# Optimization experiments

Hardware: AMD Instinct MI355X
Metric: run time of the kernel (lower is better)

Reference implementation:

```python
import jax, jax.numpy as jnp
import numpy as np

N = 50000   # nodes
E = 800000  # edges (avg degree 16)
D = 128     # dim (in == out per layer)
R = 8       # num_relations
B = 4       # num_bases
L = 2       # conv_layer_num
EPS = 1e-5      # LayerNorm eps
SLOPE = 0.2     # leaky_relu negative slope


def setup_inputs() -> dict:
    key = jax.random.key(0)
    ks = jax.random.split(key, 10)
    s = 0.05
    x = jax.random.normal(ks[0], (N, D), dtype=jnp.float32)
    edge_index = jax.random.randint(ks[1], (2, E), 0, N)
    edge_type = jax.random.randint(ks[2], (E,), 0, R)
    basis = jax.random.normal(ks[3], (L, B, D, D), dtype=jnp.float32) * s
    att_r = jax.random.normal(ks[4], (L, R, B), dtype=jnp.float32) * s
    att = jax.random.normal(ks[5], (L, 2 * D), dtype=jnp.float32) * s
    root = jax.random.normal(ks[6], (L, D, D), dtype=jnp.float32) * s
    bias = jax.random.normal(ks[7], (L, D), dtype=jnp.float32) * s
    ln_w = jnp.ones((L, D), dtype=jnp.float32)
    ln_b = jnp.zeros((L, D), dtype=jnp.float32)
    return {"x": x, "edge_index": edge_index, "edge_type": edge_type,
            "basis": basis, "att_r": att_r, "att": att, "root": root,
            "bias": bias, "ln_w": ln_w, "ln_b": ln_b}


def _gnn_layer(x, src, dst, et, basis, att_r, att, root, bias, ln_w, ln_b):
    # relation weights from bases: [R, D, D]
    w = jnp.einsum('rb,bio->rio', att_r, basis)
    # transform all nodes under all relations once, then gather per edge
    xw = jnp.einsum('ni,rio->rno', x, w)          # [R, N, D]
    x_j = xw[et, src]                              # [E, D] relation-specific src msg
    xr = x @ root                                  # [N, D] root transform
    x_i = xr[dst]                                  # [E, D]
    # attention: (cat[x_i, x_j] * att).sum(-1), leaky_relu, segment softmax by dst
    alpha = x_i @ att[:D] + x_j @ att[D:]          # [E]
    alpha = jnp.where(alpha > 0, alpha, SLOPE * alpha)
    amax = jax.ops.segment_max(alpha, dst, num_segments=N)
    amax = jnp.where(jnp.isfinite(amax), amax, 0.0)
    ex = jnp.exp(alpha - amax[dst])
    denom = jax.ops.segment_sum(ex, dst, num_segments=N)
    alpha = ex / (denom[dst] + 1e-16)
    # weighted scatter-add aggregation (dropout rate = 0 -> identity)
    aggr = jax.ops.segment_sum(x_j * alpha[:, None], dst, num_segments=N)  # [N, D]
    out = aggr + xr + bias
    # LayerNorm
    mu = out.mean(-1, keepdims=True)
    var = out.var(-1, keepdims=True)
    out = (out - mu) / jnp.sqrt(var + EPS) * ln_w + ln_b
    return jnp.tanh(out)


def reference(x, edge_index, edge_type, basis, att_r, att, root, bias, ln_w, ln_b):
    src, dst = edge_index[0], edge_index[1]
    states = []
    for l in range(L):
        x = _gnn_layer(x, src, dst, edge_type, basis[l], att_r[l], att[l],
                       root[l], bias[l], ln_w[l], ln_b[l])
        states.append(x)
    return (x, jnp.stack(states))
```

## Files before the change

kernel.cpp:

```cpp
#include <hip/hip_runtime.h>
#include <math.h>

#define D 128
#define NB 4
#define NR 8
#define NLAYER 2
#define KTOT 640
#define EPSV 1e-5f
#define SLOPE 0.2f
#define NBUK 32
#define BSHIFT 11

typedef __attribute__((ext_vector_type(8))) short short8;
typedef __attribute__((ext_vector_type(4))) float f32x4;

__device__ __forceinline__ unsigned short f2bf(float f) {
  unsigned u = __float_as_uint(f);
  u += 0x7FFF + ((u >> 16) & 1);
  return (unsigned short)(u >> 16);
}

__device__ __forceinline__ float block_sum_128(float v, volatile float* scratch) {
#pragma unroll
  for (int off = 32; off > 0; off >>= 1) v += __shfl_xor(v, off);
  __syncthreads();
  if ((threadIdx.x & 63) == 0) scratch[threadIdx.x >> 6] = v;
  __syncthreads();
  return scratch[0] + scratch[1];
}

__global__ void hist_kernel(const int* __restrict__ dst, int* __restrict__ deg, int E) {
  int e = blockIdx.x * 256 + threadIdx.x;
  if (e < E) atomicAdd(&deg[dst[e]], 1);
}

__global__ void __launch_bounds__(1024) scan_kernel(const int* __restrict__ deg,
                                                    int* __restrict__ offs,
                                                    int* __restrict__ cur,
                                                    int* __restrict__ bcur, int n) {
  __shared__ int wsums[16];
  const int tid = threadIdx.x, lane = tid & 63, wid = tid >> 6;
  int carry = 0;
  for (int base = 0; base < n; base += 4096) {
    int i0 = base + tid * 4;
    int v0 = 0, v1 = 0, v2 = 0, v3 = 0;
    if (i0 + 3 < n) {
      int4 q = *(const int4*)(deg + i0);
      v0 = q.x; v1 = q.y; v2 = q.z; v3 = q.w;
    } else if (i0 < n) {
      v0 = deg[i0];
      if (i0 + 1 < n) v1 = deg[i0 + 1];
      if (i0 + 2 < n) v2 = deg[i0 + 2];
    }
    int tsum = v0 + v1 + v2 + v3;
    int x = tsum;
#pragma unroll
    for (int off = 1; off < 64; off <<= 1) {
      int y = __shfl_up(x, off);
      if (lane >= off) x += y;
    }
    if (lane == 63) wsums[wid] = x;
    __syncthreads();
    if (wid == 0) {
      int ws = (lane < 16) ? wsums[lane] : 0;
#pragma unroll
      for (int off = 1; off < 16; off <<= 1) {
        int y = __shfl_up(ws, off);
        if (lane >= off) ws += y;
      }
      if (lane < 16) wsums[lane] = ws;
    }
    __syncthreads();
    int prefix = carry + ((wid > 0) ? wsums[wid - 1] : 0) + x - tsum;
    int e0 = prefix, e1 = e0 + v0, e2 = e1 + v1, e3 = e2 + v2;
    if (i0 < n)     { offs[i0] = e0;     cur[i0] = e0; }
    if (i0 + 1 < n) { offs[i0 + 1] = e1; cur[i0 + 1] = e1; }
    if (i0 + 2 < n) { offs[i0 + 2] = e2; cur[i0 + 2] = e2; }
    if (i0 + 3 < n) { offs[i0 + 3] = e3; cur[i0 + 3] = e3; }
    int btot = wsums[15];
    __syncthreads();
    carry += btot;
  }
  if (tid == 0) offs[n] = carry;
  __syncthreads();
  if (tid < NBUK) {
    int idx = tid << BSHIFT;
    bcur[tid * 16] = offs[idx < n ? idx : n];
  }
}

__global__ void __launch_bounds__(1024) bucket_kernel(
    const int* __restrict__ src, const int* __restrict__ dst, const int* __restrict__ et,
    int* __restrict__ bcur, unsigned long long* __restrict__ ebuf, int E) {
  __shared__ int lcnt[NBUK];
  __shared__ int lbase[NBUK];
  const int tid = threadIdx.x;
  const int e = blockIdx.x * 1024 + tid;
  if (tid < NBUK) lcnt[tid] = 0;
  __syncthreads();
  int d = 0, b = 0, rank = 0;
  unsigned pk = 0;
  bool valid = e < E;
  if (valid) {
    d = dst[e];
    pk = (unsigned)src[e] | ((unsigned)et[e] << 16);
    b = d >> BSHIFT;
    rank = atomicAdd(&lcnt[b], 1);
  }
  __syncthreads();
  if (tid < NBUK && lcnt[tid] > 0) lbase[tid] = atomicAdd(&bcur[tid * 16], lcnt[tid]);
  __syncthreads();
  if (valid) ebuf[lbase[b] + rank] = ((unsigned long long)(unsigned)d << 32) | pk;
}

__global__ void scatter2_kernel(const unsigned long long* __restrict__ ebuf,
                                int* __restrict__ cur, unsigned* __restrict__ csr, int E) {
  int e = blockIdx.x * 256 + threadIdx.x;
  if (e < E) {
    unsigned long long r = ebuf[e];
    int d = (int)(r >> 32);
    int pos = atomicAdd(&cur[d], 1);
    csr[pos] = (unsigned)r;
  }
}

__global__ void __launch_bounds__(128) prep_w(const float* __restrict__ basis,
                                              const float* __restrict__ root,
                                              const float* __restrict__ att,
                                              unsigned short* __restrict__ BT0,
                                              unsigned short* __restrict__ BT1,
                                              float* __restrict__ av0, float* __restrict__ av1) {
  __shared__ float scratch[2];
  int k = blockIdx.x, l = 0;
  if (k >= KTOT) { k -= KTOT; l = 1; }
  const float* basis_l = basis + (size_t)l * NB * D * D;
  const float* root_l  = root + (size_t)l * D * D;
  const float* att_l   = att + (size_t)l * 2 * D;
  unsigned short* BT = l ? BT1 : BT0;
  float* av = l ? av1 : av0;
  const int o = threadIdx.x;
  float v = (k < 512) ? basis_l[(size_t)(k >> 7) * (D * D) + (size_t)(k & 127) * D + o]
                      : root_l[(size_t)(k - 512) * D + o];
  BT[(size_t)o * KTOT + k] = f2bf(v);
  float w = (k < 512) ? att_l[D + o] : att_l[o];
  float s = block_sum_128(v * w, scratch);
  if (o == 0) av[k] = s;
}

__global__ void __launch_bounds__(256) prep_xa(const float* __restrict__ x0,
                                               const float* __restrict__ av,
                                               unsigned short* __restrict__ ga,
                                               float* __restrict__ ai,
                                               float* __restrict__ ajb, int N, int Npad) {
  int n = blockIdx.x * 4 + (threadIdx.x >> 6);
  int lane = threadIdx.x & 63;
  if (n >= Npad) return;
  if (n >= N) {
    *(unsigned*)(ga + (size_t)n * KTOT + 512 + 2 * lane) = 0;
    return;
  }
  float2 xv = *(const float2*)(x0 + (size_t)n * D + 2 * lane);
  unsigned packed = (unsigned)f2bf(xv.x) | ((unsigned)f2bf(xv.y) << 16);
  *(unsigned*)(ga + (size_t)n * KTOT + 512 + 2 * lane) = packed;
  float d[5];
#pragma unroll
  for (int b = 0; b < 4; ++b) {
    float2 w = *(const float2*)(av + b * D + 2 * lane);
    d[b] = xv.x * w.x + xv.y * w.y;
  }
  {
    float2 w = *(const float2*)(av + 512 + 2 * lane);
    d[4] = xv.x * w.x + xv.y * w.y;
  }
#pragma unroll
  for (int off = 1; off < 64; off <<= 1) {
#pragma unroll
    for (int i = 0; i < 5; ++i) d[i] += __shfl_xor(d[i], off);
  }
  if (lane == 0) {
    *(float4*)(ajb + (size_t)n * 4) = make_float4(d[0], d[1], d[2], d[3]);
    ai[n] = d[4];
  }
}

__global__ void __launch_bounds__(256) a2_kernel(const unsigned short* __restrict__ ga,
                                                 const float* __restrict__ av,
                                                 float* __restrict__ ai,
                                                 float* __restrict__ ajb, int N) {
  int n = blockIdx.x * 4 + (threadIdx.x >> 6);
  int lane = threadIdx.x & 63;
  if (n >= N) return;
  unsigned xv = *(const unsigned*)(ga + (size_t)n * KTOT + 512 + 2 * lane);
  float x0 = __uint_as_float(xv << 16);
  float x1 = __uint_as_float(xv & 0xFFFF0000u);
  float d[5];
#pragma unroll
  for (int b = 0; b < 4; ++b) {
    float2 w = *(const float2*)(av + b * D + 2 * lane);
    d[b] = x0 * w.x + x1 * w.y;
  }
  {
    float2 w = *(const float2*)(av + 512 + 2 * lane);
    d[4] = x0 * w.x + x1 * w.y;
  }
#pragma unroll
  for (int off = 1; off < 64; off <<= 1) {
#pragma unroll
    for (int i = 0; i < 5; ++i) d[i] += __shfl_xor(d[i], off);
  }
  if (lane == 0) {
    *(float4*)(ajb + (size_t)n * 4) = make_float4(d[0], d[1], d[2], d[3]);
    ai[n] = d[4];
  }
}

__global__ void __launch_bounds__(256) node_flash(
    unsigned short* __restrict__ ga, const float* __restrict__ ai, const float* __restrict__ ajb,
    const int* __restrict__ offs, const unsigned* __restrict__ csr,
    const float* __restrict__ attr_l, int N) {
  __shared__ float s_c[NR * NB];
  __shared__ float4 s_wc[4][64];
  __shared__ unsigned s_pk[4][64];
  const int w = threadIdx.x >> 6, lane = threadIdx.x & 63;
  const int n = blockIdx.x * 4 + w;
  if (lane < NR * NB) s_c[lane] = attr_l[lane];
  if (n >= N) return;
  const int b0 = offs[n], b1 = offs[n + 1];
  const float ain = ai[n];
  float m = -INFINITY, ssum = 0.f;
  float acc[4][2] = {};
  for (int cb = b0; cb < b1; cb += 64) {
    int cnt = min(64, b1 - cb);
    float alpha = -INFINITY;
    unsigned pk = 0;
    float4 cv = make_float4(0.f, 0.f, 0.f, 0.f);
    if (lane < cnt) {
      pk = csr[cb + lane];
      unsigned sn = pk & 0xFFFFu, rt = pk >> 16;
      float4 aj = *(const float4*)(ajb + (size_t)sn * 4);
      cv = *(const float4*)(&s_c[rt * 4]);
      float a = ain + cv.x * aj.x + cv.y * aj.y + cv.z * aj.z + cv.w * aj.w;
      alpha = a > 0.f ? a : SLOPE * a;
    }
    float cmax = alpha;
#pragma unroll
    for (int off = 32; off > 0; off >>= 1) cmax = fmaxf(cmax, __shfl_xor(cmax, off));
    float nm = fmaxf(m, cmax);
    float ex = (lane < cnt) ? __expf(alpha - nm) : 0.f;
    float csum = ex;
#pragma unroll
    for (int off = 32; off > 0; off >>= 1) csum += __shfl_xor(csum, off);
    float f = __expf(m - nm);
    ssum = ssum * f + csum;
#pragma unroll
    for (int b = 0; b < 4; ++b) { acc[b][0] *= f; acc[b][1] *= f; }
    m = nm;
    s_pk[w][lane] = pk;
    s_wc[w][lane] = make_float4(ex * cv.x, ex * cv.y, ex * cv.z, ex * cv.w);
#pragma unroll 2
    for (int j = 0; j < cnt; ++j) {
      float4 wc = s_wc[w][j];
      unsigned sn = s_pk[w][j] & 0xFFFFu;
      unsigned xv = *(const unsigned*)(ga + (size_t)sn * KTOT + 512 + 2 * lane);
      float x0 = __uint_as_float(xv << 16);
      float x1 = __uint_as_float(xv & 0xFFFF0000u);
      acc[0][0] = fmaf(wc.x, x0, acc[0][0]); acc[0][1] = fmaf(wc.x, x1, acc[0][1]);
      acc[1][0] = fmaf(wc.y, x0, acc[1][0]); acc[1][1] = fmaf(wc.y, x1, acc[1][1]);
      acc[2][0] = fmaf(wc.z, x0, acc[2][0]); acc[2][1] = fmaf(wc.z, x1, acc[2][1]);
      acc[3][0] = fmaf(wc.w, x0, acc[3][0]); acc[3][1] = fmaf(wc.w, x1, acc[3][1]);
    }
  }
  float inv = 1.f / (ssum + 1e-16f);
  unsigned short* gp = ga + (size_t)n * KTOT;
#pragma unroll
  for (int b = 0; b < 4; ++b) {
    unsigned r = (unsigned)f2bf(acc[b][0] * inv) | ((unsigned)f2bf(acc[b][1] * inv) << 16);
    *(unsigned*)(gp + b * D + 2 * lane) = r;
  }
}

__global__ void __launch_bounds__(512) gemm2_kernel(
    unsigned short* __restrict__ ga, const unsigned short* __restrict__ BT,
    const float* __restrict__ bias_l, const float* __restrict__ lnw_l,
    const float* __restrict__ lnb_l, float* __restrict__ st,
    float* __restrict__ xfinal, int n_nodes) {
  __shared__ unsigned short sB[128 * 72];
  const int tid = threadIdx.x;
  const int wv = tid >> 6, lane = tid & 63;
  const int l15 = lane & 15, quad = lane >> 4;
  const int rowb = blockIdx.x * 128 + wv * 16;
  const unsigned short* garow = ga + (size_t)(rowb + l15) * KTOT;
  f32x4 acc[8];
  const f32x4 zero = {0.f, 0.f, 0.f, 0.f};
#pragma unroll
  for (int ct = 0; ct < 8; ++ct) acc[ct] = zero;
#pragma unroll
  for (int ch = 0; ch < 10; ++ch) {
    const int k0 = ch * 64;
    short8 a[2];
#pragma unroll
    for (int kc = 0; kc < 2; ++kc)
      a[kc] = *(const short8*)(garow + k0 + kc * 32 + quad * 8);
    __syncthreads();
#pragma unroll
    for (int p = 0; p < 2; ++p) {
      int idx = p * 512 + tid;
      int col = idx >> 3, k8 = idx & 7;
      *(short8*)(sB + col * 72 + k8 * 8) =
          *(const short8*)(BT + (size_t)col * KTOT + k0 + k8 * 8);
    }
    __syncthreads();
#pragma unroll
    for (int kc = 0; kc < 2; ++kc) {
#pragma unroll
      for (int ct = 0; ct < 8; ++ct) {
        const short8* b = (const short8*)(sB + (ct * 16 + l15) * 72 + kc * 32 + quad * 8);
        acc[ct] = __builtin_amdgcn_mfma_f32_16x16x32_bf16(a[kc], *b, acc[ct], 0, 0, 0);
      }
    }
  }
  const int r0 = rowb + quad * 4;
  float bia[8], lw[8], lb[8];
#pragma unroll
  for (int ct = 0; ct < 8; ++ct) {
    int col = ct * 16 + l15;
    bia[ct] = bias_l[col]; lw[ct] = lnw_l[col]; lb[ct] = lnb_l[col];
  }
  float vsum[4] = {0.f, 0.f, 0.f, 0.f}, vsq[4] = {0.f, 0.f, 0.f, 0.f};
#pragma unroll
  for (int ct = 0; ct < 8; ++ct) {
#pragma unroll
    for (int r = 0; r < 4; ++r) {
      float v = acc[ct][r] + bia[ct];
      acc[ct][r] = v;
      vsum[r] += v; vsq[r] += v * v;
    }
  }
#pragma unroll
  for (int r = 0; r < 4; ++r) {
#pragma unroll
    for (int off = 1; off < 16; off <<= 1) {
      vsum[r] += __shfl_xor(vsum[r], off);
      vsq[r]  += __shfl_xor(vsq[r], off);
    }
  }
  float mu[4], rs[4];
#pragma unroll
  for (int r = 0; r < 4; ++r) {
    mu[r] = vsum[r] * (1.0f / D);
    float var = vsq[r] * (1.0f / D) - mu[r] * mu[r];
    rs[r] = rsqrtf(var + EPSV);
  }
#pragma unroll
  for (int ct = 0; ct < 8; ++ct) {
#pragma unroll
    for (int r = 0; r < 4; ++r) {
      int row = r0 + r;
      if (row >= n_nodes) continue;
      int col = ct * 16 + l15;
      float nv = (acc[ct][r] - mu[r]) * rs[r] * lw[ct] + lb[ct];
      float val = tanhf(nv);
      st[(size_t)row * D + col] = val;
      if (xfinal) xfinal[(size_t)row * D + col] = val;
      ga[(size_t)row * KTOT + 512 + col] = f2bf(val);
    }
  }
}

extern "C" void kernel_launch(void* const* d_in, const int* in_sizes, int n_in,
                              void* d_out, int out_size, void* d_ws, size_t ws_size,
                              hipStream_t stream) {
  const float* x0    = (const float*)d_in[0];
  const int*   ei    = (const int*)d_in[1];
  const int*   etype = (const int*)d_in[2];
  const float* basis = (const float*)d_in[3];
  const float* att_r = (const float*)d_in[4];
  const float* att   = (const float*)d_in[5];
  const float* root  = (const float*)d_in[6];
  const float* bias  = (const float*)d_in[7];
  const float* lnw   = (const float*)d_in[8];
  const float* lnb   = (const float*)d_in[9];
  float* out = (float*)d_out;
  const int N = in_sizes[0] / D;
  const int E = in_sizes[2];
  const int Npad = ((N + 127) / 128) * 128;

  char* p = (char*)d_ws;
  auto alloc = [&](size_t bytes) { void* r = (void*)p; p += (bytes + 255) & ~(size_t)255; return r; };
  unsigned short*     ga   = (unsigned short*)alloc((size_t)Npad * KTOT * 2);
  unsigned short*     BT0  = (unsigned short*)alloc((size_t)D * KTOT * 2);
  unsigned short*     BT1  = (unsigned short*)alloc((size_t)D * KTOT * 2);
  float*              av0  = (float*)alloc((size_t)KTOT * 4);
  float*              av1  = (float*)alloc((size_t)KTOT * 4);
  float*              ai   = (float*)alloc((size_t)N * 4);
  float*              ajb  = (float*)alloc((size_t)N * 4 * 4);
  int*                deg  = (int*)alloc((size_t)N * 4);
  int*                offs = (int*)alloc((size_t)(N + 1) * 4);
  int*                cur  = (int*)alloc((size_t)N * 4);
  int*                bcur = (int*)alloc((size_t)NBUK * 16 * 4);
  unsigned*           csr  = (unsigned*)alloc((size_t)E * 4);
  unsigned long long* ebuf = (unsigned long long*)alloc((size_t)E * 8);

  const int* srcp = ei;
  const int* dstp = ei + E;

  hipMemsetAsync(deg, 0, (size_t)N * 4, stream);
  hist_kernel<<<(E + 255) / 256, 256, 0, stream>>>(dstp, deg, E);
  scan_kernel<<<1, 1024, 0, stream>>>(deg, offs, cur, bcur, N);
  bucket_kernel<<<(E + 1023) / 1024, 1024, 0, stream>>>(srcp, dstp, etype, bcur, ebuf, E);
  scatter2_kernel<<<(E + 255) / 256, 256, 0, stream>>>(ebuf, cur, csr, E);

  prep_w<<<2 * KTOT, 128, 0, stream>>>(basis, root, att, BT0, BT1, av0, av1);
  prep_xa<<<Npad / 4, 256, 0, stream>>>(x0, av0, ga, ai, ajb, N, Npad);

  float* states = out + (size_t)N * D;
  for (int l = 0; l < NLAYER; ++l) {
    const unsigned short* BT_l = l ? BT1 : BT0;
    if (l > 0)
      a2_kernel<<<(N + 3) / 4, 256, 0, stream>>>(ga, av1, ai, ajb, N);
    node_flash<<<(N + 3) / 4, 256, 0, stream>>>(ga, ai, ajb, offs, csr,
                                                att_r + (size_t)l * NR * NB, N);
    float* st = states + (size_t)l * N * D;
    gemm2_kernel<<<Npad / 128, 512, 0, stream>>>(ga, BT_l, bias + (size_t)l * D,
                                                 lnw + (size_t)l * D, lnb + (size_t)l * D,
                                                 st, (l == NLAYER - 1) ? out : nullptr, N);
  }
}
```

Measured before the change: 418.0 us.

## Process four nodes per wavefront in node_flash with 16-lane groups and uint4 gathers

```diff
diff --git a/kernel.cpp b/kernel.cpp
--- a/kernel.cpp
+++ b/kernel.cpp
@@ -222,60 +222,82 @@
   __shared__ float4 s_wc[4][64];
   __shared__ unsigned s_pk[4][64];
   const int w = threadIdx.x >> 6, lane = threadIdx.x & 63;
-  const int n = blockIdx.x * 4 + w;
+  const int g = lane >> 4, s = lane & 15;
+  const int n = blockIdx.x * 16 + w * 4 + g;
   if (lane < NR * NB) s_c[lane] = attr_l[lane];
-  if (n >= N) return;
-  const int b0 = offs[n], b1 = offs[n + 1];
-  const float ain = ai[n];
-  float m = -INFINITY, ssum = 0.f;
-  float acc[4][2] = {};
-  for (int cb = b0; cb < b1; cb += 64) {
-    int cnt = min(64, b1 - cb);
-    float alpha = -INFINITY;
+  int b0 = 0, b1 = 0;
+  float ain = 0.f;
+  if (n < N) { b0 = offs[n]; b1 = offs[n + 1]; ain = ai[n]; }
+  float ssum = 0.f;
+  float acc[4][8];
+#pragma unroll
+  for (int b = 0; b < 4; ++b)
+#pragma unroll
+    for (int d = 0; d < 8; ++d) acc[b][d] = 0.f;
+
+  int nch = (b1 - b0 + 15) >> 4;
+  nch = max(nch, __shfl_xor(nch, 16));
+  nch = max(nch, __shfl_xor(nch, 32));
+
+  for (int ch = 0; ch < nch; ++ch) {
+    const int cb = b0 + (ch << 4);
+    const int cnt = min(16, b1 - cb);
+    float ex = 0.f;
+    float4 wc = make_float4(0.f, 0.f, 0.f, 0.f);
     unsigned pk = 0;
-    float4 cv = make_float4(0.f, 0.f, 0.f, 0.f);
-    if (lane < cnt) {
-      pk = csr[cb + lane];
+    if (s < cnt) {
+      pk = csr[cb + s];
       unsigned sn = pk & 0xFFFFu, rt = pk >> 16;
       float4 aj = *(const float4*)(ajb + (size_t)sn * 4);
-      cv = *(const float4*)(&s_c[rt * 4]);
+      float4 cv = *(const float4*)(&s_c[rt * 4]);
       float a = ain + cv.x * aj.x + cv.y * aj.y + cv.z * aj.z + cv.w * aj.w;
-      alpha = a > 0.f ? a : SLOPE * a;
-    }
-    float cmax = alpha;
-#pragma unroll
-    for (int off = 32; off > 0; off >>= 1) cmax = fmaxf(cmax, __shfl_xor(cmax, off));
-    float nm = fmaxf(m, cmax);
-    float ex = (lane < cnt) ? __expf(alpha - nm) : 0.f;
-    float csum = ex;
-#pragma unroll
-    for (int off = 32; off > 0; off >>= 1) csum += __shfl_xor(csum, off);
-    float f = __expf(m - nm);
-    ssum = ssum * f + csum;
-#pragma unroll
-    for (int b = 0; b < 4; ++b) { acc[b][0] *= f; acc[b][1] *= f; }
-    m = nm;
+      a = fmaxf(a, SLOPE * a);
+      ex = __expf(a);
+      ssum += ex;
+      wc = make_float4(ex * cv.x, ex * cv.y, ex * cv.z, ex * cv.w);
+    }
     s_pk[w][lane] = pk;
-    s_wc[w][lane] = make_float4(ex * cv.x, ex * cv.y, ex * cv.z, ex * cv.w);
+    s_wc[w][lane] = wc;
+    int cc = max(cnt, 0);
+    cc = max(cc, __shfl_xor(cc, 16));
+    cc = max(cc, __shfl_xor(cc, 32));
+    const float4* wrow = &s_wc[w][g * 16];
+    const unsigned* prow = &s_pk[w][g * 16];
 #pragma unroll 2
-    for (int j = 0; j < cnt; ++j) {
-      float4 wc = s_wc[w][j];
-      unsigned sn = s_pk[w][j] & 0xFFFFu;
-      unsigned xv = *(const unsigned*)(ga + (size_t)sn * KTOT + 512 + 2 * lane);
-      float x0 = __uint_as_float(xv << 16);
-      float x1 = __uint_as_float(xv & 0xFFFF0000u);
-      acc[0][0] = fmaf(wc.x, x0, acc[0][0]); acc[0][1] = fmaf(wc.x, x1, acc[0][1]);
-      acc[1][0] = fmaf(wc.y, x0, acc[1][0]); acc[1][1] = fmaf(wc.y, x1, acc[1][1]);
-      acc[2][0] = fmaf(wc.z, x0, acc[2][0]); acc[2][1] = fmaf(wc.z, x1, acc[2][1]);
-      acc[3][0] = fmaf(wc.w, x0, acc[3][0]); acc[3][1] = fmaf(wc.w, x1, acc[3][1]);
-    }
-  }
-  float inv = 1.f / (ssum + 1e-16f);
-  unsigned short* gp = ga + (size_t)n * KTOT;
-#pragma unroll
-  for (int b = 0; b < 4; ++b) {
-    unsigned r = (unsigned)f2bf(acc[b][0] * inv) | ((unsigned)f2bf(acc[b][1] * inv) << 16);
-    *(unsigned*)(gp + b * D + 2 * lane) = r;
+    for (int j = 0; j < cc; ++j) {
+      float4 wcj = wrow[j];
+      unsigned sn = prow[j] & 0xFFFFu;
+      const uint4 q = *(const uint4*)(ga + sn * (unsigned)KTOT + 512u + (unsigned)s * 8u);
+      float xl, xh;
+#define ACC8(K, QQ)                                           \
+      xl = __uint_as_float((QQ) << 16);                       \
+      xh = __uint_as_float((QQ) & 0xFFFF0000u);               \
+      acc[0][2*K]   = fmaf(wcj.x, xl, acc[0][2*K]);           \
+      acc[0][2*K+1] = fmaf(wcj.x, xh, acc[0][2*K+1]);         \
+      acc[1][2*K]   = fmaf(wcj.y, xl, acc[1][2*K]);           \
+      acc[1][2*K+1] = fmaf(wcj.y, xh, acc[1][2*K+1]);         \
+      acc[2][2*K]   = fmaf(wcj.z, xl, acc[2][2*K]);           \
+      acc[2][2*K+1] = fmaf(wcj.z, xh, acc[2][2*K+1]);         \
+      acc[3][2*K]   = fmaf(wcj.w, xl, acc[3][2*K]);           \
+      acc[3][2*K+1] = fmaf(wcj.w, xh, acc[3][2*K+1]);
+      ACC8(0, q.x) ACC8(1, q.y) ACC8(2, q.z) ACC8(3, q.w)
+#undef ACC8
+    }
+  }
+#pragma unroll
+  for (int off = 1; off < 16; off <<= 1) ssum += __shfl_xor(ssum, off);
+  if (n < N) {
+    const float inv = 1.f / (ssum + 1e-16f);
+    unsigned short* gp = ga + (size_t)n * KTOT;
+#pragma unroll
+    for (int b = 0; b < 4; ++b) {
+      uint4 r;
+      r.x = (unsigned)f2bf(acc[b][0] * inv) | ((unsigned)f2bf(acc[b][1] * inv) << 16);
+      r.y = (unsigned)f2bf(acc[b][2] * inv) | ((unsigned)f2bf(acc[b][3] * inv) << 16);
+      r.z = (unsigned)f2bf(acc[b][4] * inv) | ((unsigned)f2bf(acc[b][5] * inv) << 16);
+      r.w = (unsigned)f2bf(acc[b][6] * inv) | ((unsigned)f2bf(acc[b][7] * inv) << 16);
+      *(uint4*)(gp + b * D + s * 8) = r;
+    }
   }
 }
 
@@ -418,8 +440,8 @@
     const unsigned short* BT_l = l ? BT1 : BT0;
     if (l > 0)
       a2_kernel<<<(N + 3) / 4, 256, 0, stream>>>(ga, av1, ai, ajb, N);
-    node_flash<<<(N + 3) / 4, 256, 0, stream>>>(ga, ai, ajb, offs, csr,
-                                                att_r + (size_t)l * NR * NB, N);
+    node_flash<<<(N + 15) / 16, 256, 0, stream>>>(ga, ai, ajb, offs, csr,
+                                                  att_r + (size_t)l * NR * NB, N);
     float* st = states + (size_t)l * N * D;
     gemm2_kernel<<<Npad / 128, 512, 0, stream>>>(ga, BT_l, bias + (size_t)l * D,
                                                  lnw + (size_t)l * D, lnb + (size_t)l * D,
```

Result: no change. 415.1 us (-0.7%).
